# Kernel tuning notes

Measured on AMD Instinct MI355X. Metric: run time of the kernel, lower is better.

Reference implementation:

```python
import jax, jax.numpy as jnp
import numpy as np

TAU = 0.5
EPS = 1e-12


def _projection(z, W1, b1, W2, b2):
    # fc2(elu(fc1(z)))
    h = jax.nn.elu(z @ W1 + b1)
    return h @ W2 + b2


def _l2_normalize(z):
    n = jnp.linalg.norm(z, axis=1, keepdims=True)
    return z / jnp.maximum(n, EPS)


def _semi_loss(h1, h2, tau):
    n1 = _l2_normalize(h1)
    n2 = _l2_normalize(h2)
    refl = jnp.exp((n1 @ n1.T) / tau)      # [N, N]
    between = jnp.exp((n1 @ n2.T) / tau)   # [N, N]
    denom = refl.sum(axis=1) + between.sum(axis=1) - jnp.diagonal(refl)
    return -jnp.log(jnp.diagonal(between) / denom)


def setup_inputs() -> dict:
    key = jax.random.key(0)
    k1, k2, k3, k4 = jax.random.split(key, 4)
    N, H, P = 12288, 256, 256
    s = 1.0 / np.sqrt(H)
    return {
        "z1": jax.random.normal(k1, (N, H), dtype=jnp.float32),
        "z2": jax.random.normal(k2, (N, H), dtype=jnp.float32),
        "W1": jax.random.normal(k3, (H, P), dtype=jnp.float32) * s,
        "b1": jnp.zeros((P,), dtype=jnp.float32),
        "W2": jax.random.normal(k4, (P, H), dtype=jnp.float32) * s,
        "b2": jnp.zeros((H,), dtype=jnp.float32),
    }


def reference(z1, z2, W1, b1, W2, b2):
    h1 = _projection(z1, W1, b1, W2, b2)
    h2 = _projection(z2, W1, b1, W2, b2)
    l1 = _semi_loss(h1, h2, TAU)
    l2 = _semi_loss(h2, h1, TAU)
    return ((l1 + l2) * 0.5).mean()
```

## Files before the change

### kernel.cpp

```cpp
#include <hip/hip_runtime.h>
#include <hip/hip_bf16.h>

typedef __attribute__((ext_vector_type(4))) float f32x4;
typedef __attribute__((ext_vector_type(8))) short bf16x8;

#define NR 12288
#define HD 256
#define TAU 0.5f
#define NU 24576
#define NTT 192
#define NSUB 384
#define NBLK (NTT * (NTT + 1) / 2)
#define LAM 1.69864368f

__device__ __forceinline__ unsigned short f2bf(float f) {
    unsigned int x = __builtin_bit_cast(unsigned int, f);
    x += 0x7fffu + ((x >> 16) & 1u);
    return (unsigned short)(x >> 16);
}

__device__ __forceinline__ unsigned char f2e4m3(float f) {
    unsigned int u = __builtin_bit_cast(unsigned int, f);
    unsigned int s = (u >> 24) & 0x80u;
    float af = fabsf(f);
    if (af >= 464.f) return (unsigned char)(s | 0x7Eu);
    if (af < 0.015625f) {
        unsigned int q = (unsigned int)(af * 512.f + 0.5f);
        return (unsigned char)(s | q);
    }
    int e = (int)((u >> 23) & 0xffu) - 127;
    unsigned int mant = u & 0x7fffffu;
    unsigned int val = (unsigned int)((e + 7) << 3) | (mant >> 20);
    unsigned int rem = mant & 0xfffffu;
    val += (rem > 0x80000u) || (rem == 0x80000u && (val & 1u));
    return (unsigned char)(s | val);
}

__device__ __forceinline__ float row16_sum(float x) {
    int v;
    v = __builtin_amdgcn_update_dpp(0, __builtin_bit_cast(int, x), 0xB1, 0xF, 0xF, true);
    x += __builtin_bit_cast(float, v);
    v = __builtin_amdgcn_update_dpp(0, __builtin_bit_cast(int, x), 0x4E, 0xF, 0xF, true);
    x += __builtin_bit_cast(float, v);
    v = __builtin_amdgcn_update_dpp(0, __builtin_bit_cast(int, x), 0x141, 0xF, 0xF, true);
    x += __builtin_bit_cast(float, v);
    v = __builtin_amdgcn_update_dpp(0, __builtin_bit_cast(int, x), 0x140, 0xF, 0xF, true);
    x += __builtin_bit_cast(float, v);
    return x;
}

__device__ __forceinline__ bf16x8 cvt8(const float* __restrict__ p) {
    float4 a = *(const float4*)p;
    float4 b = *(const float4*)(p + 4);
    union { unsigned int i[4]; bf16x8 v; } u;
    u.i[0] = ((unsigned int)f2bf(a.y) << 16) | f2bf(a.x);
    u.i[1] = ((unsigned int)f2bf(a.w) << 16) | f2bf(a.z);
    u.i[2] = ((unsigned int)f2bf(b.y) << 16) | f2bf(b.x);
    u.i[3] = ((unsigned int)f2bf(b.w) << 16) | f2bf(b.z);
    return u.v;
}

__global__ __launch_bounds__(256) void transpose_cast_kernel(const float* __restrict__ W1,
                                                             const float* __restrict__ W2,
                                                             unsigned short* __restrict__ W1t,
                                                             unsigned short* __restrict__ W2t) {
    const float* W = blockIdx.y ? W2 : W1;
    unsigned short* Wt = blockIdx.y ? W2t : W1t;
    int n = blockIdx.x;
    int k = threadIdx.x;
    Wt[n * HD + k] = f2bf(W[k * HD + n]);
}

__global__ __launch_bounds__(256) void projA_kernel(const float* __restrict__ z1,
                                                    const float* __restrict__ z2,
                                                    const unsigned short* __restrict__ W1t,
                                                    const float* __restrict__ b1,
                                                    unsigned short* __restrict__ t1,
                                                    unsigned short* __restrict__ t2) {
    const float* A = blockIdx.y ? z2 : z1;
    unsigned short* C = blockIdx.y ? t2 : t1;
    const int lane = threadIdx.x & 63;
    const int wave = threadIdx.x >> 6;
    const int row0 = blockIdx.x * 64;
    const int col0 = wave * 64;
    const int lr = lane & 15, lk = lane >> 4;

    f32x4 acc[4][4] = {};
    const unsigned short* Bb = W1t + (size_t)(col0 + lr) * HD + lk * 8;
#pragma unroll
    for (int k0 = 0; k0 < HD; k0 += 32) {
        bf16x8 af[4], bfr[4];
#pragma unroll
        for (int m = 0; m < 4; ++m)
            af[m] = cvt8(A + (size_t)(row0 + m * 16 + lr) * HD + k0 + lk * 8);
#pragma unroll
        for (int n = 0; n < 4; ++n) bfr[n] = *(const bf16x8*)(Bb + n * 16 * HD + k0);
#pragma unroll
        for (int m = 0; m < 4; ++m)
#pragma unroll
            for (int n = 0; n < 4; ++n)
                acc[m][n] = __builtin_amdgcn_mfma_f32_16x16x32_bf16(af[m], bfr[n], acc[m][n], 0, 0, 0);
    }
#pragma unroll
    for (int m = 0; m < 4; ++m) {
#pragma unroll
        for (int n = 0; n < 4; ++n) {
            int col = col0 + n * 16 + lr;
            float b = b1[col];
#pragma unroll
            for (int r = 0; r < 4; ++r) {
                int row = row0 + m * 16 + lk * 4 + r;
                float v = acc[m][n][r] + b;
                v = v > 0.f ? v : expm1f(v);
                C[(size_t)row * HD + col] = f2bf(v);
            }
        }
    }
}

__global__ __launch_bounds__(256) void projB_kernel(const unsigned short* __restrict__ t1,
                                                    const unsigned short* __restrict__ t2,
                                                    const unsigned short* __restrict__ W2t,
                                                    const float* __restrict__ b2,
                                                    float* __restrict__ h1,
                                                    float* __restrict__ h2) {
    const unsigned short* A = blockIdx.y ? t2 : t1;
    float* C = blockIdx.y ? h2 : h1;
    const int lane = threadIdx.x & 63;
    const int wave = threadIdx.x >> 6;
    const int row0 = blockIdx.x * 64;
    const int col0 = wave * 64;
    const int lr = lane & 15, lk = lane >> 4;

    f32x4 acc[4][4] = {};
    const unsigned short* Ab = A + (size_t)(row0 + lr) * HD + lk * 8;
    const unsigned short* Bb = W2t + (size_t)(col0 + lr) * HD + lk * 8;
#pragma unroll
    for (int k0 = 0; k0 < HD; k0 += 32) {
        bf16x8 af[4], bfr[4];
#pragma unroll
        for (int m = 0; m < 4; ++m) af[m] = *(const bf16x8*)(Ab + m * 16 * HD + k0);
#pragma unroll
        for (int n = 0; n < 4; ++n) bfr[n] = *(const bf16x8*)(Bb + n * 16 * HD + k0);
#pragma unroll
        for (int m = 0; m < 4; ++m)
#pragma unroll
            for (int n = 0; n < 4; ++n)
                acc[m][n] = __builtin_amdgcn_mfma_f32_16x16x32_bf16(af[m], bfr[n], acc[m][n], 0, 0, 0);
    }
#pragma unroll
    for (int m = 0; m < 4; ++m) {
#pragma unroll
        for (int n = 0; n < 4; ++n) {
            int col = col0 + n * 16 + lr;
            float b = b2[col];
#pragma unroll
            for (int r = 0; r < 4; ++r) {
                int row = row0 + m * 16 + lk * 4 + r;
                C[(size_t)row * HD + col] = acc[m][n][r] + b;
            }
        }
    }
}

__global__ __launch_bounds__(256) void norm_diag_kernel(const float* __restrict__ h1,
                                                        const float* __restrict__ h2,
                                                        unsigned char* __restrict__ n1,
                                                        unsigned char* __restrict__ n2,
                                                        float* __restrict__ dvec) {
    const int lane = threadIdx.x & 63;
    const int wave = threadIdx.x >> 6;
    const int row = blockIdx.x * 4 + wave;
    const float4 a = *(const float4*)(h1 + (size_t)row * HD + lane * 4);
    const float4 b = *(const float4*)(h2 + (size_t)row * HD + lane * 4);
    float sa = a.x * a.x + a.y * a.y + a.z * a.z + a.w * a.w;
    float sb = b.x * b.x + b.y * b.y + b.z * b.z + b.w * b.w;
    float sab = a.x * b.x + a.y * b.y + a.z * b.z + a.w * b.w;
#pragma unroll
    for (int m = 32; m; m >>= 1) {
        sa += __shfl_xor(sa, m);
        sb += __shfl_xor(sb, m);
        sab += __shfl_xor(sab, m);
    }
    float na = sqrtf(sa); na = na > 1e-12f ? na : 1e-12f;
    float nb = sqrtf(sb); nb = nb > 1e-12f ? nb : 1e-12f;
    float ia = 1.f / na, ib = 1.f / nb;
    float sca = ia * LAM, scb = ib * LAM;
    uchar4 q1, q2;
    q1.x = f2e4m3(a.x * sca); q1.y = f2e4m3(a.y * sca); q1.z = f2e4m3(a.z * sca); q1.w = f2e4m3(a.w * sca);
    q2.x = f2e4m3(b.x * scb); q2.y = f2e4m3(b.y * scb); q2.z = f2e4m3(b.z * scb); q2.w = f2e4m3(b.w * scb);
    const int sw = ((row >> 3) & 1) << 3;
    *(uchar4*)(n1 + (size_t)row * HD + ((lane * 4) ^ sw)) = q1;
    *(uchar4*)(n2 + (size_t)row * HD + ((lane * 4) ^ sw)) = q2;
    if (lane == 0) dvec[row] = sab * ia * ib * (1.f / TAU);
}

__global__ __launch_bounds__(256, 2) void gram_kernel(const unsigned char* __restrict__ nU8,
                                                      float* __restrict__ RPART) {
    __shared__ __align__(16) unsigned char lA[128 * 256];
    __shared__ __align__(16) unsigned char lB[128 * 256];

    const int bid = blockIdx.x;
    const int t0 = (bid & 7) * (NBLK / 8) + (bid >> 3);
    int i = (int)((385.f - sqrtf((float)(385 * 385 - 8 * t0))) * 0.5f);
    if (i < 0) i = 0;
    if (i > NTT - 1) i = NTT - 1;
    while (i > 0 && i * NTT - i * (i - 1) / 2 > t0) --i;
    while ((i + 1) * NTT - (i + 1) * i / 2 <= t0) ++i;
    const int j = i + (t0 - (i * NTT - i * (i - 1) / 2));
    const bool diag = (i == j);

    const unsigned char* X = nU8 + (size_t)i * 128 * HD;
    const unsigned char* Y = nU8 + (size_t)j * 128 * HD;

    const int t = threadIdx.x;
    const int lane = t & 63;
    const int wave = t >> 6;
    const int wr = wave >> 1, wc = wave & 1;
    const int lr = lane & 15, lk = lane >> 4;

    {
        const int rbase = t >> 4;
        const int schunk = (t & 15) ^ rbase;
        const unsigned char* gx = X + rbase * 256 + schunk * 16;
        const unsigned char* gy = Y + rbase * 256 + schunk * 16;
#pragma unroll
        for (int c = 0; c < 8; ++c) {
            __builtin_amdgcn_global_load_lds(
                (const __attribute__((address_space(1))) unsigned int*)(gx + c * 4096),
                (__attribute__((address_space(3))) unsigned int*)(&lA[c * 4096 + t * 16]),
                16, 0, 0);
        }
        if (!diag) {
#pragma unroll
            for (int c = 0; c < 8; ++c) {
                __builtin_amdgcn_global_load_lds(
                    (const __attribute__((address_space(1))) unsigned int*)(gy + c * 4096),
                    (__attribute__((address_space(3))) unsigned int*)(&lB[c * 4096 + t * 16]),
                    16, 0, 0);
            }
        }
    }
    __syncthreads();

    f32x4 acc[4][4] = {};
    const int hswap = (lr >> 3) & 1;
    const unsigned char* sA = lA + (size_t)(wr * 64 + lr) * 256 + ((lk & 1) ^ hswap) * 8;
    const unsigned char* sBb = (diag ? lA : lB);
    const unsigned char* sB = sBb + (size_t)(wc * 64 + lr) * 256 + ((lk & 1) ^ hswap) * 8;

    const unsigned char* pA[8];
    const unsigned char* pB[8];
#pragma unroll
    for (int ks = 0; ks < 8; ++ks) {
        const int chnk = ((2 * ks + (lk >> 1)) ^ lr) * 16;
        pA[ks] = sA + chnk;
        pB[ks] = sB + chnk;
    }

#pragma unroll
    for (int ks = 0; ks < 8; ++ks) {
        long af[4], bfr[4];
#pragma unroll
        for (int m = 0; m < 4; ++m)
            af[m] = *(const long*)(pA[ks] + m * 16 * 256);
#pragma unroll
        for (int n = 0; n < 4; ++n)
            bfr[n] = *(const long*)(pB[ks] + n * 16 * 256);
#pragma unroll
        for (int m = 0; m < 4; ++m)
#pragma unroll
            for (int n = 0; n < 4; ++n)
                acc[m][n] = __builtin_amdgcn_mfma_f32_16x16x32_fp8_fp8(af[m], bfr[n], acc[m][n], 0, 0, 0);
    }

#pragma unroll
    for (int m = 0; m < 4; ++m)
#pragma unroll
        for (int n = 0; n < 4; ++n)
#pragma unroll
            for (int r = 0; r < 4; ++r)
                acc[m][n][r] = exp2f(acc[m][n][r]);

    {
        float* dst = RPART + (size_t)(2 * j + wc) * NU + i * 128 + wr * 64;
#pragma unroll
        for (int m = 0; m < 4; ++m) {
#pragma unroll
            for (int r = 0; r < 4; ++r) {
                float rs = (acc[m][0][r] + acc[m][1][r]) + (acc[m][2][r] + acc[m][3][r]);
                rs = row16_sum(rs);
                if (lr == 0) dst[m * 16 + lk * 4 + r] = rs;
            }
        }
    }
    if (!diag) {
        float* dst = RPART + (size_t)(2 * i + wr) * NU + j * 128 + wc * 64;
#pragma unroll
        for (int n = 0; n < 4; ++n) {
            float cs = 0.f;
#pragma unroll
            for (int m = 0; m < 4; ++m)
#pragma unroll
                for (int r = 0; r < 4; ++r) cs += acc[m][n][r];
            cs += __shfl_xor(cs, 16);
            cs += __shfl_xor(cs, 32);
            if (lk == 0) dst[n * 16 + lr] = cs;
        }
    }
}

__global__ __launch_bounds__(128) void loss_sum_kernel(const float* __restrict__ RPART,
                                                       const float* __restrict__ dvec,
                                                       float* __restrict__ partial) {
    const int i = blockIdx.x * 128 + threadIdx.x;
    float s1 = 0.f, s2 = 0.f;
#pragma unroll 8
    for (int p = 0; p < NSUB; ++p) {
        s1 += RPART[(size_t)p * NU + i];
        s2 += RPART[(size_t)p * NU + NR + i];
    }
    const float e2 = 7.389056099f;
    float v = 0.5f * (logf(s1 - e2) + logf(s2 - e2)) - dvec[i];
#pragma unroll
    for (int m = 32; m; m >>= 1) v += __shfl_xor(v, m);
    __shared__ float wsum[2];
    if ((threadIdx.x & 63) == 0) wsum[threadIdx.x >> 6] = v;
    __syncthreads();
    if (threadIdx.x == 0) partial[blockIdx.x] = wsum[0] + wsum[1];
}

__global__ __launch_bounds__(128) void loss_final_kernel(const float* __restrict__ partial,
                                                         float* __restrict__ out, int nb) {
    float s = 0.f;
    for (int i = threadIdx.x; i < nb; i += 128) s += partial[i];
#pragma unroll
    for (int m = 32; m; m >>= 1) s += __shfl_xor(s, m);
    __shared__ float wsum[2];
    if ((threadIdx.x & 63) == 0) wsum[threadIdx.x >> 6] = s;
    __syncthreads();
    if (threadIdx.x == 0) out[0] = (wsum[0] + wsum[1]) * (1.f / (float)NR);
}

extern "C" void kernel_launch(void* const* d_in, const int* in_sizes, int n_in,
                              void* d_out, int out_size, void* d_ws, size_t ws_size,
                              hipStream_t stream) {
    const float* z1 = (const float*)d_in[0];
    const float* z2 = (const float*)d_in[1];
    const float* W1 = (const float*)d_in[2];
    const float* b1 = (const float*)d_in[3];
    const float* W2 = (const float*)d_in[4];
    const float* b2 = (const float*)d_in[5];

    char* ws = (char*)d_ws;
    size_t off = 0;
    auto alloc = [&](size_t bytes) {
        void* p = ws + off;
        off += (bytes + 255) & ~(size_t)255;
        return p;
    };
    const size_t NH2 = (size_t)NR * HD * 2;
    unsigned short* t1 = (unsigned short*)alloc(NH2);
    unsigned short* t2 = (unsigned short*)alloc(NH2);
    unsigned short* W1t = (unsigned short*)alloc(HD * HD * 2);
    unsigned short* W2t = (unsigned short*)alloc(HD * HD * 2);
    float* h1 = (float*)alloc((size_t)NR * HD * 4);
    float* h2 = (float*)alloc((size_t)NR * HD * 4);
    unsigned char* nU = (unsigned char*)alloc((size_t)NU * HD);
    float* dvec = (float*)alloc(NR * 4);
    float* partial = (float*)alloc(96 * 4);
    float* RPART = (float*)ws;

    transpose_cast_kernel<<<dim3(HD, 2), 256, 0, stream>>>(W1, W2, W1t, W2t);

    projA_kernel<<<dim3(NR / 64, 2), 256, 0, stream>>>(z1, z2, W1t, b1, t1, t2);
    projB_kernel<<<dim3(NR / 64, 2), 256, 0, stream>>>(t1, t2, W2t, b2, h1, h2);

    norm_diag_kernel<<<NR / 4, 256, 0, stream>>>(h1, h2, nU, nU + (size_t)NR * HD, dvec);

    gram_kernel<<<NBLK, 256, 0, stream>>>(nU, RPART);

    loss_sum_kernel<<<NR / 128, 128, 0, stream>>>(RPART, dvec, partial);
    loss_final_kernel<<<1, 128, 0, stream>>>(partial, (float*)d_out, NR / 128);
}
```

Measured before the change: 275.5 us.

## Split gram tile K loads into two halves to overlap MFMA with loads

The shared-memory layout of the fp8 gram tiles is reorganized into two K-halves of 128 bytes per row, each with its own XOR swizzle. Loads for both halves are issued up front. A partial vmcnt wait plus barrier lets the MFMAs on the first half start while the second half is still in flight. This hides part of the global-to-LDS load latency, at the cost of more complex addressing and hand-written waitcnt counts that must match the number of issued loads.

```diff
diff --git a/kernel.cpp b/kernel.cpp
--- a/kernel.cpp
+++ b/kernel.cpp
@@ -197,8 +197,8 @@
 
 __global__ __launch_bounds__(256, 2) void gram_kernel(const unsigned char* __restrict__ nU8,
                                                       float* __restrict__ RPART) {
-    __shared__ __align__(16) unsigned char lA[128 * 256];
-    __shared__ __align__(16) unsigned char lB[128 * 256];
+    __shared__ __align__(16) unsigned char lA[2 * 128 * 128];
+    __shared__ __align__(16) unsigned char lB[2 * 128 * 128];
 
     const int bid = blockIdx.x;
     const int t0 = (bid & 7) * (NBLK / 8) + (bid >> 3);
@@ -220,53 +220,91 @@
     const int lr = lane & 15, lk = lane >> 4;
 
     {
-        const int rbase = t >> 4;
-        const int schunk = (t & 15) ^ rbase;
-        const unsigned char* gx = X + rbase * 256 + schunk * 16;
-        const unsigned char* gy = Y + rbase * 256 + schunk * 16;
-#pragma unroll
-        for (int c = 0; c < 8; ++c) {
+        const int rbase = t >> 3;
+        const int sch = ((t & 7) ^ (rbase & 7)) * 16;
+        const unsigned char* gx = X + rbase * 256 + sch;
+        const unsigned char* gy = Y + rbase * 256 + sch;
+#pragma unroll
+        for (int c = 0; c < 4; ++c) {
             __builtin_amdgcn_global_load_lds(
-                (const __attribute__((address_space(1))) unsigned int*)(gx + c * 4096),
+                (const __attribute__((address_space(1))) unsigned int*)(gx + c * 8192),
                 (__attribute__((address_space(3))) unsigned int*)(&lA[c * 4096 + t * 16]),
                 16, 0, 0);
         }
         if (!diag) {
 #pragma unroll
-            for (int c = 0; c < 8; ++c) {
+            for (int c = 0; c < 4; ++c) {
                 __builtin_amdgcn_global_load_lds(
-                    (const __attribute__((address_space(1))) unsigned int*)(gy + c * 4096),
+                    (const __attribute__((address_space(1))) unsigned int*)(gy + c * 8192),
                     (__attribute__((address_space(3))) unsigned int*)(&lB[c * 4096 + t * 16]),
                     16, 0, 0);
             }
         }
-    }
-    __syncthreads();
+#pragma unroll
+        for (int c = 0; c < 4; ++c) {
+            __builtin_amdgcn_global_load_lds(
+                (const __attribute__((address_space(1))) unsigned int*)(gx + 128 + c * 8192),
+                (__attribute__((address_space(3))) unsigned int*)(&lA[16384 + c * 4096 + t * 16]),
+                16, 0, 0);
+        }
+        if (!diag) {
+#pragma unroll
+            for (int c = 0; c < 4; ++c) {
+                __builtin_amdgcn_global_load_lds(
+                    (const __attribute__((address_space(1))) unsigned int*)(gy + 128 + c * 8192),
+                    (__attribute__((address_space(3))) unsigned int*)(&lB[16384 + c * 4096 + t * 16]),
+                    16, 0, 0);
+            }
+        }
+    }
+    if (diag) asm volatile("s_waitcnt vmcnt(4)" ::: "memory");
+    else      asm volatile("s_waitcnt vmcnt(8)" ::: "memory");
+    __builtin_amdgcn_s_barrier();
 
     f32x4 acc[4][4] = {};
     const int hswap = (lr >> 3) & 1;
-    const unsigned char* sA = lA + (size_t)(wr * 64 + lr) * 256 + ((lk & 1) ^ hswap) * 8;
+    const unsigned char* sA = lA + (size_t)(wr * 64 + lr) * 128 + ((lk & 1) ^ hswap) * 8;
     const unsigned char* sBb = (diag ? lA : lB);
-    const unsigned char* sB = sBb + (size_t)(wc * 64 + lr) * 256 + ((lk & 1) ^ hswap) * 8;
+    const unsigned char* sB = sBb + (size_t)(wc * 64 + lr) * 128 + ((lk & 1) ^ hswap) * 8;
 
     const unsigned char* pA[8];
     const unsigned char* pB[8];
 #pragma unroll
     for (int ks = 0; ks < 8; ++ks) {
-        const int chnk = ((2 * ks + (lk >> 1)) ^ lr) * 16;
-        pA[ks] = sA + chnk;
-        pB[ks] = sB + chnk;
-    }
-
-#pragma unroll
-    for (int ks = 0; ks < 8; ++ks) {
+        const int src = 2 * ks + (lk >> 1);
+        const int off = (src >> 3) * 16384 + (((src & 7) ^ (lr & 7)) * 16);
+        pA[ks] = sA + off;
+        pB[ks] = sB + off;
+    }
+
+#pragma unroll
+    for (int ks = 0; ks < 4; ++ks) {
         long af[4], bfr[4];
 #pragma unroll
         for (int m = 0; m < 4; ++m)
-            af[m] = *(const long*)(pA[ks] + m * 16 * 256);
+            af[m] = *(const long*)(pA[ks] + m * 2048);
 #pragma unroll
         for (int n = 0; n < 4; ++n)
-            bfr[n] = *(const long*)(pB[ks] + n * 16 * 256);
+            bfr[n] = *(const long*)(pB[ks] + n * 2048);
+#pragma unroll
+        for (int m = 0; m < 4; ++m)
+#pragma unroll
+            for (int n = 0; n < 4; ++n)
+                acc[m][n] = __builtin_amdgcn_mfma_f32_16x16x32_fp8_fp8(af[m], bfr[n], acc[m][n], 0, 0, 0);
+    }
+
+    asm volatile("s_waitcnt vmcnt(0)" ::: "memory");
+    __builtin_amdgcn_s_barrier();
+
+#pragma unroll
+    for (int ks = 4; ks < 8; ++ks) {
+        long af[4], bfr[4];
+#pragma unroll
+        for (int m = 0; m < 4; ++m)
+            af[m] = *(const long*)(pA[ks] + m * 2048);
+#pragma unroll
+        for (int n = 0; n < 4; ++n)
+            bfr[n] = *(const long*)(pB[ks] + n * 2048);
 #pragma unroll
         for (int m = 0; m < 4; ++m)
 #pragma unroll
```

After: 275.5 us. Within noise of the previous version (-0.0%).

## Load gram A-operand straight from global into registers, halving LDS use

Applied to the files above, without the earlier changes.

The A tile of the fp8 Gram kernel no longer goes through shared memory. Each lane reads its MFMA A fragments directly from global memory, reusing the existing swizzled layout, and prefetches the next k-step one iteration ahead. Only the B tile is staged in LDS, so shared memory per block halves and launch bounds rise from 2 to 4 blocks per CU. The cost is narrow 8-byte global loads that are less coalesced, whose latency is only partly hidden by the one-step prefetch.

```diff
diff --git a/kernel.cpp b/kernel.cpp
--- a/kernel.cpp
+++ b/kernel.cpp
@@ -195,9 +195,8 @@
     if (lane == 0) dvec[row] = sab * ia * ib * (1.f / TAU);
 }
 
-__global__ __launch_bounds__(256, 2) void gram_kernel(const unsigned char* __restrict__ nU8,
+__global__ __launch_bounds__(256, 4) void gram_kernel(const unsigned char* __restrict__ nU8,
                                                       float* __restrict__ RPART) {
-    __shared__ __align__(16) unsigned char lA[128 * 256];
     __shared__ __align__(16) unsigned char lB[128 * 256];
 
     const int bid = blockIdx.x;
@@ -218,60 +217,52 @@
     const int wave = t >> 6;
     const int wr = wave >> 1, wc = wave & 1;
     const int lr = lane & 15, lk = lane >> 4;
+    const int hswap = (lr >> 3) & 1;
 
     {
         const int rbase = t >> 4;
         const int schunk = (t & 15) ^ rbase;
-        const unsigned char* gx = X + rbase * 256 + schunk * 16;
-        const unsigned char* gy = Y + rbase * 256 + schunk * 16;
+        const unsigned char* gy = (diag ? X : Y) + rbase * 256 + schunk * 16;
 #pragma unroll
         for (int c = 0; c < 8; ++c) {
             __builtin_amdgcn_global_load_lds(
-                (const __attribute__((address_space(1))) unsigned int*)(gx + c * 4096),
-                (__attribute__((address_space(3))) unsigned int*)(&lA[c * 4096 + t * 16]),
+                (const __attribute__((address_space(1))) unsigned int*)(gy + c * 4096),
+                (__attribute__((address_space(3))) unsigned int*)(&lB[c * 4096 + t * 16]),
                 16, 0, 0);
         }
-        if (!diag) {
-#pragma unroll
-            for (int c = 0; c < 8; ++c) {
-                __builtin_amdgcn_global_load_lds(
-                    (const __attribute__((address_space(1))) unsigned int*)(gy + c * 4096),
-                    (__attribute__((address_space(3))) unsigned int*)(&lB[c * 4096 + t * 16]),
-                    16, 0, 0);
-            }
-        }
-    }
+    }
+
+    const unsigned char* Abase = X + (size_t)(wr * 64 + lr) * 256 + ((lk * 8) ^ (hswap * 8));
+
+    long aCur[4], aNxt[4];
+#pragma unroll
+    for (int m = 0; m < 4; ++m)
+        aCur[m] = *(const long*)(Abase + m * 16 * 256);
+
     __syncthreads();
 
     f32x4 acc[4][4] = {};
-    const int hswap = (lr >> 3) & 1;
-    const unsigned char* sA = lA + (size_t)(wr * 64 + lr) * 256 + ((lk & 1) ^ hswap) * 8;
-    const unsigned char* sBb = (diag ? lA : lB);
-    const unsigned char* sB = sBb + (size_t)(wc * 64 + lr) * 256 + ((lk & 1) ^ hswap) * 8;
-
-    const unsigned char* pA[8];
-    const unsigned char* pB[8];
+    const unsigned char* sB = lB + (size_t)(wc * 64 + lr) * 256 + ((lk & 1) ^ hswap) * 8;
+
 #pragma unroll
     for (int ks = 0; ks < 8; ++ks) {
+        if (ks < 7) {
+#pragma unroll
+            for (int m = 0; m < 4; ++m)
+                aNxt[m] = *(const long*)(Abase + m * 16 * 256 + (ks + 1) * 32);
+        }
         const int chnk = ((2 * ks + (lk >> 1)) ^ lr) * 16;
-        pA[ks] = sA + chnk;
-        pB[ks] = sB + chnk;
-    }
-
-#pragma unroll
-    for (int ks = 0; ks < 8; ++ks) {
-        long af[4], bfr[4];
+        long bfr[4];
+#pragma unroll
+        for (int n = 0; n < 4; ++n)
+            bfr[n] = *(const long*)(sB + n * 16 * 256 + chnk);
 #pragma unroll
         for (int m = 0; m < 4; ++m)
-            af[m] = *(const long*)(pA[ks] + m * 16 * 256);
-#pragma unroll
-        for (int n = 0; n < 4; ++n)
-            bfr[n] = *(const long*)(pB[ks] + n * 16 * 256);
-#pragma unroll
-        for (int m = 0; m < 4; ++m)
 #pragma unroll
             for (int n = 0; n < 4; ++n)
-                acc[m][n] = __builtin_amdgcn_mfma_f32_16x16x32_fp8_fp8(af[m], bfr[n], acc[m][n], 0, 0, 0);
+                acc[m][n] = __builtin_amdgcn_mfma_f32_16x16x32_fp8_fp8(aCur[m], bfr[n], acc[m][n], 0, 0, 0);
+#pragma unroll
+        for (int m = 0; m < 4; ++m) aCur[m] = aNxt[m];
     }
 
 #pragma unroll
```

Measured after the change: 387.6 us. +40.7%, slower.
